# Performance work log

Hardware: AMD Instinct MI355X
Metric: run time of the kernel (lower is better)

The kernel has to match this reference:

```python
import jax, jax.numpy as jnp
import numpy as np

K_PERIODS = 6


def setup_inputs() -> dict:
    key = jax.random.key(0)
    x = jax.random.normal(key, (16, 2048, 128), dtype=jnp.float32)
    return {"x": x}


def reference(x):
    # x: [B, T, N] -> out: [B, K, Pmax, N].
    # Pmax is data-dependent in the torch original (max selected period); here we
    # use the static upper bound Pmax = T so shapes are jit-static. Columns
    # p >= P_row are zero, matching the original's zero padding.
    B, T, N = x.shape
    BN = B * N
    seqs = jnp.transpose(x, (0, 2, 1)).reshape(BN, T)  # [BN, T]

    # --- top-k nonzero frequencies by spectral energy ---
    spec = jnp.fft.rfft(seqs, axis=-1)
    mag2 = spec.real ** 2 + spec.imag ** 2
    mag2 = mag2.at[:, 0].set(0.0)  # kill DC bin
    k = min(K_PERIODS, mag2.shape[-1] - 1)
    _, kidx = jax.lax.top_k(mag2, k)          # [BN, K]
    kidx = jnp.maximum(kidx, 1)

    # --- per-(row, freq) period geometry ---
    P = jnp.maximum(T // kidx, 1)             # [BN, K] period length
    cycles = jnp.maximum(T // P, 1)           # [BN, K] number of full cycles
    take = cycles * P
    base = jnp.maximum(T - take, 0)           # [BN, K] start offset

    # --- fold-and-average via scatter-add (no [BN,K,Cmax,Pmax] blowup) ---
    # element at time t >= base maps to phase p = (t - base) % P, averaged over cycles
    t = jnp.arange(T, dtype=jnp.int32)
    rel = t[None, None, :] - base[:, :, None]          # [BN, K, T]
    valid = rel >= 0
    p = jnp.where(valid, rel % P[:, :, None], 0)       # phase index in [0, P)
    vals = jnp.where(valid, seqs[:, None, :], 0.0)     # [BN, K, T]

    row = jnp.arange(BN * k, dtype=jnp.int32).reshape(BN, k, 1)
    seg_ids = row * T + p                               # flat segment id
    sums = jax.ops.segment_sum(vals.reshape(-1), seg_ids.reshape(-1),
                               num_segments=BN * k * T)
    seg = sums.reshape(BN, k, T) / cycles[:, :, None].astype(vals.dtype)

    out = seg.reshape(B, N, k, T).transpose(0, 2, 3, 1)  # [B, K, Pmax=T, N]
    return out
```

## Files before the change

kernel.cpp:

```cpp
#include <hip/hip_runtime.h>
#include <stdint.h>

#define TB   256
#define TLEN 2048
#define NB   16
#define NCH  128
#define BN   (NB*NCH)
#define KP   6

typedef unsigned long long u64;

__device__ inline float2 cmul(float2 a, float2 b) {
  return make_float2(a.x * b.x - a.y * b.y, a.x * b.y + a.y * b.x);
}
__device__ inline float2 cadd(float2 a, float2 b) { return make_float2(a.x + b.x, a.y + b.y); }
__device__ inline float2 csub(float2 a, float2 b) { return make_float2(a.x - b.x, a.y - b.y); }
__device__ inline float2 cmni(float2 a) { return make_float2(a.y, -a.x); }

#define PAD(o) ((o) + ((o) >> 4))
#define C2 0.70710678118654752f

__device__ inline void radix8(const float2 A[8], float2 w1, float2 B[8]) {
  float2 s02 = cadd(A[0], A[4]), d02 = csub(A[0], A[4]);
  float2 s13 = cadd(A[2], A[6]), d13 = csub(A[2], A[6]);
  float2 E0 = cadd(s02, s13), E1 = cadd(d02, cmni(d13));
  float2 E2 = csub(s02, s13), E3 = csub(d02, cmni(d13));
  float2 t02 = cadd(A[1], A[5]), e02 = csub(A[1], A[5]);
  float2 t13 = cadd(A[3], A[7]), e13 = csub(A[3], A[7]);
  float2 O0 = cadd(t02, t13), O1 = cadd(e02, cmni(e13));
  float2 O2 = csub(t02, t13), O3 = csub(e02, cmni(e13));
  float2 T0 = O0;
  float2 T1 = make_float2(C2 * (O1.x + O1.y), C2 * (O1.y - O1.x));
  float2 T2 = cmni(O2);
  float2 T3 = make_float2(C2 * (O3.y - O3.x), -C2 * (O3.x + O3.y));
  float2 b0 = cadd(E0, T0), b4 = csub(E0, T0);
  float2 b1 = cadd(E1, T1), b5 = csub(E1, T1);
  float2 b2 = cadd(E2, T2), b6 = csub(E2, T2);
  float2 b3 = cadd(E3, T3), b7 = csub(E3, T3);
  float2 w2 = cmul(w1, w1);
  float2 w3 = cmul(w2, w1);
  float2 w4 = cmul(w2, w2);
  float2 w5 = cmul(w4, w1);
  float2 w6 = cmul(w4, w2);
  float2 w7 = cmul(w4, w3);
  B[0] = b0;
  B[1] = cmul(w1, b1);
  B[2] = cmul(w2, b2);
  B[3] = cmul(w3, b3);
  B[4] = cmul(w4, b4);
  B[5] = cmul(w5, b5);
  B[6] = cmul(w6, b6);
  B[7] = cmul(w7, b7);
}

__global__ __launch_bounds__(256) void k_fft_fold(const float* __restrict__ x,
                                                  float* __restrict__ seg,
                                                  int* __restrict__ Pg) {
  __shared__ __align__(16) float2 bufA[2176];
  __shared__ __align__(16) float2 bufB[2176];
  __shared__ float sraw[2][TLEN];
  __shared__ float2 tw[256];
  __shared__ u64 wmax[4];
  __shared__ int4 prm[2][KP];
  int tid = threadIdx.x, lane = tid & 63, wv = tid >> 6;
  int r0 = blockIdx.x * 2;
  int b = r0 >> 7, n0 = r0 & 127;

  const float2* x2 = (const float2*)x;
  size_t xoff = (size_t)b * TLEN * 64 + (n0 >> 1);
#pragma unroll
  for (int kk = 0; kk < 8; kk++) {
    int t = tid + kk * TB;
    float2 v = x2[xoff + (size_t)t * 64];
    sraw[0][t] = v.x;
    sraw[1][t] = v.y;
  }
  {
    float sn, cs;
    sincosf((-6.283185307179586f / 2048.f) * (float)tid, &sn, &cs);
    tw[tid] = make_float2(cs, sn);
  }
  __syncthreads();

  {
    int i = tid;
    float2 A[8], B[8];
#pragma unroll
    for (int j = 0; j < 8; j++)
      A[j] = make_float2(sraw[0][i + j * 256], sraw[1][i + j * 256]);
    radix8(A, tw[i], B);
    int o = 8 * i;
#pragma unroll
    for (int j = 0; j < 8; j++) bufA[PAD(o + j)] = B[j];
  }
#pragma unroll
  for (int stage = 0; stage < 2; stage++) {
    int s = stage == 0 ? 8 : 64;
    float2* xb = stage == 0 ? bufA : bufB;
    float2* yb = stage == 0 ? bufB : bufA;
    __syncthreads();
    int i = tid;
    int q = i & (s - 1);
    int cb = i - q;
    float2 A[8], B[8];
#pragma unroll
    for (int j = 0; j < 8; j++) A[j] = xb[PAD(i + j * 256)];
    radix8(A, tw[cb], B);
    int o = q + 8 * cb;
#pragma unroll
    for (int j = 0; j < 8; j++) yb[PAD(o + j * s)] = B[j];
  }
  __syncthreads();
#pragma unroll
  for (int ii = 0; ii < 2; ii++) {
    int i = tid + ii * TB;
    float2 a0 = bufA[PAD(i)], a1 = bufA[PAD(i + 512)];
    float2 a2 = bufA[PAD(i + 1024)], a3 = bufA[PAD(i + 1536)];
    float2 S02 = cadd(a0, a2), D02 = csub(a0, a2);
    float2 S13 = cadd(a1, a3), D13 = csub(a1, a3);
    bufB[PAD(i)]        = cadd(S02, S13);
    bufB[PAD(i + 512)]  = cadd(D02, cmni(D13));
    bufB[PAD(i + 1024)] = csub(S02, S13);
    bufB[PAD(i + 1536)] = csub(D02, cmni(D13));
  }
  __syncthreads();

  const float2* Z = bufB;
  u64* keys = (u64*)bufA;
  for (int i = tid; i < 1024; i += TB) {
    int kb = i + 1;
    float2 zk = Z[PAD(kb)];
    float2 zc = Z[PAD(2048 - kb)];
    float ax = zk.x + zc.x, ay = zk.y - zc.y;
    float bx = zk.x - zc.x, by = zk.y + zc.y;
    float m2a = ax * ax + ay * ay;
    float m2b = bx * bx + by * by;
    keys[i]        = ((u64)__float_as_uint(m2a) << 32) | (unsigned)(0xFFFFFFFFu - (unsigned)kb);
    keys[1024 + i] = ((u64)__float_as_uint(m2b) << 32) | (unsigned)(0xFFFFFFFFu - (unsigned)kb);
  }
  __syncthreads();

  int rw2 = wv >> 1;
  u64* kb2 = keys + rw2 * 1024;
  int t2 = tid & 127;
  for (int r = 0; r < KP; r++) {
    u64 best = 0ull;
    for (int i = t2; i < 1024; i += 128) {
      u64 v = kb2[i];
      best = v > best ? v : best;
    }
    for (int off = 32; off > 0; off >>= 1) {
      u64 o = __shfl_down(best, off);
      best = o > best ? o : best;
    }
    if (lane == 0) wmax[wv] = best;
    __syncthreads();
    if (t2 == 0) {
      u64 b0 = wmax[rw2 * 2], b1 = wmax[rw2 * 2 + 1];
      best = b0 > b1 ? b0 : b1;
      int bin = (int)(0xFFFFFFFFu - (unsigned)(best & 0xFFFFFFFFull));
      if (bin < 1 || bin > 1024) bin = 1;
      kb2[bin - 1] = 0ull;
      int P = TLEN / bin;
      int cyc = TLEN / P;
      int base = TLEN - cyc * P;
      prm[rw2][r] = make_int4(P, base, cyc, 0);
      Pg[(r0 + rw2) * KP + r] = P;
    }
    __syncthreads();
  }

  for (int task = wv; task < 2 * KP; task += 4) {
    int rw = task & 1, k = task >> 1;
    int4 pr = prm[rw][k];
    int P = pr.x, base = pr.y, cyc = pr.z;
    float inv = 1.0f / (float)cyc;
    const float* srow = sraw[rw];
    float* dst = seg + ((size_t)(r0 + rw) * KP + k) * TLEN;

    if (P >= 64) {
      for (int p = lane; p < P; p += 64) {
        const float* sp = srow + base + p;
        float s = 0.f;
        for (int c = 0; c < cyc; c++) s += sp[c * P];
        dst[p] = s * inv;
      }
    } else {
      int wc = 64 / P, u = wc * P, ci = lane / P;
      float v = 0.f;
      if (lane < u) {
        for (int c0 = 0; c0 < cyc; c0 += wc) {
          int c = c0 + ci;
          if (c < cyc) v += srow[base + c0 * P + lane];
        }
      }
      for (int s = P; s < u; s <<= 1) {
        float o = __shfl_down(v, s);
        if (lane + s < u) v += o;
      }
      if (lane < P) dst[lane] = v * inv;
    }
  }
}

__global__ __launch_bounds__(256) void k_expand(const float* __restrict__ seg,
                                                const int* __restrict__ Pg,
                                                float4* __restrict__ out4) {
  __shared__ int Parr[NCH];
  int z = blockIdx.x;
  int pc = z & 15, bk = z >> 4;
  int b = bk / KP, k = bk - KP * b;
  int tid = threadIdx.x;
  if (tid < NCH) Parr[tid] = Pg[(b * NCH + tid) * KP + k];
  __syncthreads();
  int p0 = pc * 128;
  for (int e = tid; e < 4096; e += TB) {
    int p = p0 + (e >> 5);
    int n4 = (e & 31) * 4;
    float4 v = make_float4(0.f, 0.f, 0.f, 0.f);
    float* vp = &v.x;
#pragma unroll
    for (int c = 0; c < 4; c++) {
      int n = n4 + c;
      if (p < Parr[n])
        vp[c] = seg[((size_t)(b * NCH + n) * KP + k) * TLEN + p];
    }
    out4[((size_t)bk * TLEN + p) * (NCH / 4) + (e & 31)] = v;
  }
}

extern "C" void kernel_launch(void* const* d_in, const int* in_sizes, int n_in,
                              void* d_out, int out_size, void* d_ws, size_t ws_size,
                              hipStream_t stream) {
  const float* x = (const float*)d_in[0];
  float* out = (float*)d_out;
  char* ws = (char*)d_ws;

  const size_t seg_bytes = (size_t)BN * KP * TLEN * 4;
  float* seg = (float*)ws;
  int* Pg = (int*)(ws + seg_bytes);

  k_fft_fold<<<BN / 2, 256, 0, stream>>>(x, seg, Pg);
  k_expand<<<NB * KP * 16, 256, 0, stream>>>(seg, Pg, (float4*)out);
}
```

Baseline: 164.5 us.

## Add transpose kernel, shrink FFT LDS footprint, and skip loads in zero region of expand

Adds a separate tiled transpose kernel so the FFT kernel reads contiguous rows instead of strided 8-byte gathers from x. The FFT kernel drops its raw-sample shared buffer, folds the first radix-8 stage into the generic loop, reloads raw rows from global into bufB after the spectrum is consumed, and adds an occupancy hint of 4 blocks per CU. The expand kernel computes the max period per (b,k) and writes zeros without reading seg for tiles past it. This costs an extra kernel launch and an extra round trip of the input through global memory.

```diff
diff --git a/kernel.cpp b/kernel.cpp
--- a/kernel.cpp
+++ b/kernel.cpp
@@ -53,51 +53,50 @@
   B[7] = cmul(w7, b7);
 }
 
-__global__ __launch_bounds__(256) void k_fft_fold(const float* __restrict__ x,
-                                                  float* __restrict__ seg,
-                                                  int* __restrict__ Pg) {
+__global__ __launch_bounds__(256) void k_transpose(const float* __restrict__ x,
+                                                   float* __restrict__ seqs) {
+  __shared__ float tile[64][65];
+  int bid = blockIdx.x;
+  int tb = bid & 31, nb = (bid >> 5) & 1, b = bid >> 6;
+  int t0 = tb * 64, n0 = nb * 64;
+  int tx = threadIdx.x & 63, ty = threadIdx.x >> 6;
+#pragma unroll
+  for (int tt = ty; tt < 64; tt += 4)
+    tile[tt][tx] = x[(size_t)(b * TLEN + t0 + tt) * NCH + n0 + tx];
+  __syncthreads();
+#pragma unroll
+  for (int nn = ty; nn < 64; nn += 4)
+    seqs[(size_t)(b * NCH + n0 + nn) * TLEN + t0 + tx] = tile[tx][nn];
+}
+
+__global__ __launch_bounds__(256, 4) void k_fft_fold(const float* __restrict__ seqs,
+                                                     float* __restrict__ seg,
+                                                     int* __restrict__ Pg) {
   __shared__ __align__(16) float2 bufA[2176];
   __shared__ __align__(16) float2 bufB[2176];
-  __shared__ float sraw[2][TLEN];
   __shared__ float2 tw[256];
   __shared__ u64 wmax[4];
   __shared__ int4 prm[2][KP];
   int tid = threadIdx.x, lane = tid & 63, wv = tid >> 6;
   int r0 = blockIdx.x * 2;
-  int b = r0 >> 7, n0 = r0 & 127;
-
-  const float2* x2 = (const float2*)x;
-  size_t xoff = (size_t)b * TLEN * 64 + (n0 >> 1);
+  const float* row0 = seqs + (size_t)r0 * TLEN;
+
 #pragma unroll
   for (int kk = 0; kk < 8; kk++) {
     int t = tid + kk * TB;
-    float2 v = x2[xoff + (size_t)t * 64];
-    sraw[0][t] = v.x;
-    sraw[1][t] = v.y;
+    bufA[PAD(t)] = make_float2(row0[t], row0[t + TLEN]);
   }
   {
     float sn, cs;
     sincosf((-6.283185307179586f / 2048.f) * (float)tid, &sn, &cs);
-    tw[tid] = make_float2(cs, sn);
-  }
-  __syncthreads();
-
-  {
-    int i = tid;
-    float2 A[8], B[8];
-#pragma unroll
-    for (int j = 0; j < 8; j++)
-      A[j] = make_float2(sraw[0][i + j * 256], sraw[1][i + j * 256]);
-    radix8(A, tw[i], B);
-    int o = 8 * i;
-#pragma unroll
-    for (int j = 0; j < 8; j++) bufA[PAD(o + j)] = B[j];
-  }
-#pragma unroll
-  for (int stage = 0; stage < 2; stage++) {
-    int s = stage == 0 ? 8 : 64;
-    float2* xb = stage == 0 ? bufA : bufB;
-    float2* yb = stage == 0 ? bufB : bufA;
+    tw[tid & 255] = make_float2(cs, sn);
+  }
+
+#pragma unroll
+  for (int stage = 0; stage < 3; stage++) {
+    int s = (stage == 0) ? 1 : (stage == 1) ? 8 : 64;
+    float2* xb = (stage == 1) ? bufB : bufA;
+    float2* yb = (stage == 1) ? bufA : bufB;
     __syncthreads();
     int i = tid;
     int q = i & (s - 1);
@@ -114,29 +113,44 @@
 #pragma unroll
   for (int ii = 0; ii < 2; ii++) {
     int i = tid + ii * TB;
-    float2 a0 = bufA[PAD(i)], a1 = bufA[PAD(i + 512)];
-    float2 a2 = bufA[PAD(i + 1024)], a3 = bufA[PAD(i + 1536)];
+    float2 a0 = bufB[PAD(i)], a1 = bufB[PAD(i + 512)];
+    float2 a2 = bufB[PAD(i + 1024)], a3 = bufB[PAD(i + 1536)];
     float2 S02 = cadd(a0, a2), D02 = csub(a0, a2);
     float2 S13 = cadd(a1, a3), D13 = csub(a1, a3);
-    bufB[PAD(i)]        = cadd(S02, S13);
-    bufB[PAD(i + 512)]  = cadd(D02, cmni(D13));
-    bufB[PAD(i + 1024)] = csub(S02, S13);
-    bufB[PAD(i + 1536)] = csub(D02, cmni(D13));
-  }
-  __syncthreads();
-
-  const float2* Z = bufB;
-  u64* keys = (u64*)bufA;
-  for (int i = tid; i < 1024; i += TB) {
+    bufA[PAD(i)]        = cadd(S02, S13);
+    bufA[PAD(i + 512)]  = cadd(D02, cmni(D13));
+    bufA[PAD(i + 1024)] = csub(S02, S13);
+    bufA[PAD(i + 1536)] = csub(D02, cmni(D13));
+  }
+  __syncthreads();
+
+  u64 kra[4], krb[4];
+#pragma unroll
+  for (int ii = 0; ii < 4; ii++) {
+    int i = tid + ii * TB;
     int kb = i + 1;
-    float2 zk = Z[PAD(kb)];
-    float2 zc = Z[PAD(2048 - kb)];
+    float2 zk = bufA[PAD(kb)];
+    float2 zc = bufA[PAD(2048 - kb)];
     float ax = zk.x + zc.x, ay = zk.y - zc.y;
     float bx = zk.x - zc.x, by = zk.y + zc.y;
     float m2a = ax * ax + ay * ay;
     float m2b = bx * bx + by * by;
-    keys[i]        = ((u64)__float_as_uint(m2a) << 32) | (unsigned)(0xFFFFFFFFu - (unsigned)kb);
-    keys[1024 + i] = ((u64)__float_as_uint(m2b) << 32) | (unsigned)(0xFFFFFFFFu - (unsigned)kb);
+    kra[ii] = ((u64)__float_as_uint(m2a) << 32) | (unsigned)(0xFFFFFFFFu - (unsigned)kb);
+    krb[ii] = ((u64)__float_as_uint(m2b) << 32) | (unsigned)(0xFFFFFFFFu - (unsigned)kb);
+  }
+  __syncthreads();
+  u64* keys = (u64*)bufA;
+#pragma unroll
+  for (int ii = 0; ii < 4; ii++) {
+    int i = tid + ii * TB;
+    keys[i] = kra[ii];
+    keys[1024 + i] = krb[ii];
+  }
+  {
+    const float4* s4 = (const float4*)row0;
+    float4* r4 = (float4*)bufB;
+#pragma unroll
+    for (int ii = 0; ii < 4; ii++) r4[tid + ii * TB] = s4[tid + ii * TB];
   }
   __syncthreads();
 
@@ -170,12 +184,13 @@
     __syncthreads();
   }
 
+  float* srows = (float*)bufB;
   for (int task = wv; task < 2 * KP; task += 4) {
     int rw = task & 1, k = task >> 1;
     int4 pr = prm[rw][k];
     int P = pr.x, base = pr.y, cyc = pr.z;
     float inv = 1.0f / (float)cyc;
-    const float* srow = sraw[rw];
+    const float* srow = srows + rw * TLEN;
     float* dst = seg + ((size_t)(r0 + rw) * KP + k) * TLEN;
 
     if (P >= 64) {
@@ -207,25 +222,45 @@
                                                 const int* __restrict__ Pg,
                                                 float4* __restrict__ out4) {
   __shared__ int Parr[NCH];
+  __shared__ int Pmax_s;
   int z = blockIdx.x;
   int pc = z & 15, bk = z >> 4;
   int b = bk / KP, k = bk - KP * b;
   int tid = threadIdx.x;
   if (tid < NCH) Parr[tid] = Pg[(b * NCH + tid) * KP + k];
   __syncthreads();
+  if (tid < 64) {
+    int m = max(Parr[tid], Parr[tid + 64]);
+    for (int off = 32; off > 0; off >>= 1) {
+      int o = __shfl_down(m, off);
+      m = o > m ? o : m;
+    }
+    if (tid == 0) Pmax_s = m;
+  }
+  __syncthreads();
   int p0 = pc * 128;
-  for (int e = tid; e < 4096; e += TB) {
-    int p = p0 + (e >> 5);
-    int n4 = (e & 31) * 4;
-    float4 v = make_float4(0.f, 0.f, 0.f, 0.f);
-    float* vp = &v.x;
-#pragma unroll
-    for (int c = 0; c < 4; c++) {
-      int n = n4 + c;
-      if (p < Parr[n])
-        vp[c] = seg[((size_t)(b * NCH + n) * KP + k) * TLEN + p];
-    }
-    out4[((size_t)bk * TLEN + p) * (NCH / 4) + (e & 31)] = v;
+  int Pmax = Pmax_s;
+  float4 z4 = make_float4(0.f, 0.f, 0.f, 0.f);
+  size_t obase = (size_t)bk * TLEN * (NCH / 4);
+  if (p0 >= Pmax) {
+    for (int e = tid; e < 4096; e += TB)
+      out4[obase + (size_t)(p0 + (e >> 5)) * (NCH / 4) + (e & 31)] = z4;
+  } else {
+    for (int e = tid; e < 4096; e += TB) {
+      int p = p0 + (e >> 5);
+      float4 v = z4;
+      if (p < Pmax) {
+        int n4 = (e & 31) * 4;
+        float* vp = &v.x;
+#pragma unroll
+        for (int c = 0; c < 4; c++) {
+          int n = n4 + c;
+          if (p < Parr[n])
+            vp[c] = seg[((size_t)(b * NCH + n) * KP + k) * TLEN + p];
+        }
+      }
+      out4[obase + (size_t)p * (NCH / 4) + (e & 31)] = v;
+    }
   }
 }
 
@@ -236,10 +271,13 @@
   float* out = (float*)d_out;
   char* ws = (char*)d_ws;
 
-  const size_t seg_bytes = (size_t)BN * KP * TLEN * 4;
-  float* seg = (float*)ws;
-  int* Pg = (int*)(ws + seg_bytes);
-
-  k_fft_fold<<<BN / 2, 256, 0, stream>>>(x, seg, Pg);
+  const size_t seqs_bytes = (size_t)BN * TLEN * 4;
+  const size_t seg_bytes  = (size_t)BN * KP * TLEN * 4;
+  float* seqs = (float*)ws;
+  float* seg  = (float*)(ws + seqs_bytes);
+  int* Pg     = (int*)(ws + seqs_bytes + seg_bytes);
+
+  k_transpose<<<1024, 256, 0, stream>>>(x, seqs);
+  k_fft_fold<<<BN / 2, 256, 0, stream>>>(seqs, seg, Pg);
   k_expand<<<NB * KP * 16, 256, 0, stream>>>(seg, Pg, (float4*)out);
 }
```

Result: faster. 157.8 us (-4.1%).
